# Kernel tuning notes

Hardware: AMD Instinct MI355X
Metric: run time of the kernel (lower is better)

Reference implementation:

```python
import jax, jax.numpy as jnp
import numpy as np
from math import factorial

IRREPS_IN1 = [(128, 0), (64, 1), (32, 2)]  # (mul, l): features
IRREPS_IN2 = [(1, 0), (1, 1), (1, 2)]      # spherical harmonics lmax=2
BATCH = 16384

# ---------- real Clebsch-Gordan coefficients (e3nn convention) ----------

def _su2_cg(j1, j2, j3, m1, m2, m3):
    if m3 != m1 + m2:
        return 0.0
    f = factorial
    pref = ((2 * j3 + 1) * f(j1 + j2 - j3) * f(j1 - j2 + j3) * f(-j1 + j2 + j3) / f(j1 + j2 + j3 + 1)) ** 0.5
    pref *= (f(j3 + m3) * f(j3 - m3) * f(j1 - m1) * f(j1 + m1) * f(j2 - m2) * f(j2 + m2)) ** 0.5
    s = 0.0
    for v in range(0, j1 + j2 - j3 + 1):
        a = j1 + j2 - j3 - v; b = j1 - m1 - v; c = j2 + m2 - v
        d = j3 - j2 + m1 + v; e = j3 - j1 - m2 + v
        if min(a, b, c, d, e) < 0:
            continue
        s += (-1) ** v / (f(v) * f(a) * f(b) * f(c) * f(d) * f(e))
    return pref * s


def _su2_cg_tensor(l1, l2, l3):
    C = np.zeros((2 * l1 + 1, 2 * l2 + 1, 2 * l3 + 1))
    for m1 in range(-l1, l1 + 1):
        for m2 in range(-l2, l2 + 1):
            for m3 in range(-l3, l3 + 1):
                C[l1 + m1, l2 + m2, l3 + m3] = _su2_cg(l1, l2, l3, m1, m2, m3)
    return C


def _q(l):
    # change of basis real -> complex spherical harmonics
    q = np.zeros((2 * l + 1, 2 * l + 1), dtype=np.complex128)
    for m in range(-l, 0):
        q[l + m, l + abs(m)] = 1.0 / np.sqrt(2.0)
        q[l + m, l - abs(m)] = -1j / np.sqrt(2.0)
    q[l, l] = 1.0
    for m in range(1, l + 1):
        q[l + m, l + abs(m)] = (-1) ** m / np.sqrt(2.0)
        q[l + m, l - abs(m)] = 1j * (-1) ** m / np.sqrt(2.0)
    return (-1j) ** l * q


def _real_cg(l1, l2, l3):
    C = _su2_cg_tensor(l1, l2, l3).astype(np.complex128)
    Q1, Q2, Q3 = _q(l1), _q(l2), _q(l3)
    C = np.einsum('ij,kl,mn,ikn->jlm', Q1, Q2, np.conj(Q3.T), C)
    assert np.abs(C.imag).max() < 1e-8
    return np.ascontiguousarray(C.real.astype(np.float32))

# precompute all CG tensors needed by the full tensor product
CG = {}
for _m1, _l1 in IRREPS_IN1:
    for _m2, _l2 in IRREPS_IN2:
        for _l3 in range(abs(_l1 - _l2), _l1 + _l2 + 1):
            if (_l1, _l2, _l3) not in CG:
                CG[(_l1, _l2, _l3)] = _real_cg(_l1, _l2, _l3)


def _tensor_product(x, y):
    """Full CG tensor product. x:[B,480] y:[B,9] -> dict l3 -> list of [B,mul,2l3+1]."""
    B = x.shape[0]
    outs = {}
    off1 = 0
    for mul1, l1 in IRREPS_IN1:
        d1 = 2 * l1 + 1
        x_blk = x[:, off1:off1 + mul1 * d1].reshape(B, mul1, d1)
        off1 += mul1 * d1
        off2 = 0
        for mul2, l2 in IRREPS_IN2:
            d2 = 2 * l2 + 1
            y_blk = y[:, off2:off2 + mul2 * d2].reshape(B, mul2, d2)
            off2 += mul2 * d2
            for l3 in range(abs(l1 - l2), l1 + l2 + 1):
                cg = jnp.asarray(CG[(l1, l2, l3)])  # [d1,d2,d3]
                z = jnp.einsum('ijk,bui,bvj->buvk', cg, x_blk, y_blk)
                outs.setdefault(l3, []).append(z.reshape(B, mul1 * mul2, 2 * l3 + 1))
    return outs


def setup_inputs() -> dict:
    key = jax.random.key(0)
    k = jax.random.split(key, 5)
    dim1 = sum(m * (2 * l + 1) for m, l in IRREPS_IN1)  # 480
    dim2 = sum(m * (2 * l + 1) for m, l in IRREPS_IN2)  # 9
    x = jax.random.normal(k[0], (BATCH, dim1), dtype=jnp.float32)
    y = jax.random.normal(k[1], (BATCH, dim2), dtype=jnp.float32)
    # fan-in per output l of the equivariant Linear (tp outputs with matching l)
    W0 = jax.random.normal(k[2], (224, 128), dtype=jnp.float32)
    W1 = jax.random.normal(k[3], (384, 64), dtype=jnp.float32)
    W2 = jax.random.normal(k[4], (352, 32), dtype=jnp.float32)
    return {"x": x, "y": y, "W0": W0, "W1": W1, "W2": W2}


def reference(x, y, W0, W1, W2):
    B = x.shape[0]
    outs = _tensor_product(x, y)
    Ws = {0: W0, 1: W1, 2: W2}
    res = []
    for mul_out, l in IRREPS_IN1:
        blk = jnp.concatenate(outs[l], axis=1)  # [B, tot_mul, 2l+1]
        tot_mul = blk.shape[1]
        o = jnp.einsum('bui,uv->bvi', blk, Ws[l]) / np.sqrt(tot_mul).astype(np.float32)
        res.append(o.reshape(B, mul_out * (2 * l + 1)))
    return jnp.concatenate(res, axis=1)  # [B, 480]
```

## Files before the change

kernel.cpp:

```cpp
#include <hip/hip_runtime.h>
#include <math.h>
#include <stdint.h>

#define NBATCH 16384
#define MB 16
#define NT 256
#define NBLOCKS (NBATCH/MB)
#define WT_BYTE_OFF 2560
#define XPITCH 488

typedef float  f32x4 __attribute__((ext_vector_type(4)));
typedef short  s16x8 __attribute__((ext_vector_type(8)));

__device__ const int P_CGOFF[15] = {0,1,10,35,44,53,80,125,170,245,270,315,390,415,490};
__device__ const int P_D2[15]    = {1,3,5,3,1,3,5,3,5,5,3,5,1,3,5};
__device__ const int P_D3[15]    = {1,1,1,3,3,3,3,3,3,5,5,5,5,5,5};
__device__ const int P_TSTART[15]= {0,1,4,9,12,21,30,39,54,69,74,89,104,129,154};
__device__ const int P_YOFF[15]  = {0,1,4,1,0,1,4,1,4,4,1,4,0,1,4};
__device__ const int CG_L1[15] = {0,1,2,0,1,1,1,2,2,0,1,1,2,2,2};
__device__ const int CG_L2[15] = {0,1,2,1,0,1,2,1,2,2,1,2,0,1,2};
__device__ const int CG_L3[15] = {0,0,0,1,1,1,1,1,1,2,2,2,2,2,2};

__device__ const int   SEG_WB[15] = {0,16384,24576, 28672,36864,40960,45056,49152,51200,
                                     53248,57344,59392,61440,62464,63488};
__device__ const int   SEG_SH[15] = {7,6,5, 7,6,6,6,5,5, 7,6,6,5,5,5};
__device__ const int   SEG_U0[15] = {0,128,192, 0,128,192,256,320,352, 0,128,192,256,288,320};
__device__ const int   SEG_G[15]  = {0,0,0, 1,1,1,1,1,1, 2,2,2,2,2,2};
__device__ const float SEG_SC[3]  = {0.066815310478f, 0.051031036308f, 0.053300179089f};

__device__ const float FCT[13] = {1.f,1.f,2.f,6.f,24.f,120.f,720.f,5040.f,40320.f,
                                  362880.f,3628800.f,39916800.f,479001600.f};

__device__ float su2f(int j1,int j2,int j3,int m1,int m2,int m3){
  float pref = sqrtf((float)(2*j3+1)*FCT[j1+j2-j3]*FCT[j1-j2+j3]*FCT[-j1+j2+j3]/FCT[j1+j2+j3+1]);
  pref *= sqrtf(FCT[j3+m3]*FCT[j3-m3]*FCT[j1-m1]*FCT[j1+m1]*FCT[j2-m2]*FCT[j2+m2]);
  float s = 0.f;
  for (int v=0; v<=j1+j2-j3; ++v){
    int a=j1+j2-j3-v, b=j1-m1-v, c=j2+m2-v, d=j3-j2+m1+v, e=j3-j1-m2+v;
    if (a<0||b<0||c<0||d<0||e<0) continue;
    float term = 1.f/(FCT[v]*FCT[a]*FCT[b]*FCT[c]*FCT[d]*FCT[e]);
    s += (v&1) ? -term : term;
  }
  return pref*s;
}

__device__ void qvalf(int l,int r,int c,float* qr,float* qi){
  int m = r - l;
  const float is2 = 0.70710678118654752440f;
  float br=0.f, bi=0.f;
  if (m<0){
    if (c == l - m) br = is2;
    else if (c == l + m) bi = -is2;
  } else if (m==0){
    if (c==l) br = 1.f;
  } else {
    float sg = (m&1)? -1.f : 1.f;
    if (c == l + m) br = sg*is2;
    else if (c == l - m) bi = sg*is2;
  }
  if (l==1){ float nr = bi, ni = -br; br=nr; bi=ni; }
  else if (l==2){ br=-br; bi=-bi; }
  *qr=br; *qi=bi;
}

__device__ __forceinline__ uint32_t f2bf(float f){
  uint32_t u = __float_as_uint(f);
  return (u + 0x7fffu + ((u>>16)&1u)) >> 16;
}
__device__ __forceinline__ float bf2f(uint32_t v){ return __uint_as_float(v << 16); }

__global__ void prep(const float* __restrict__ W0, const float* __restrict__ W1,
                     const float* __restrict__ W2, float* __restrict__ ws)
{
  int t = blockIdx.x*NT + threadIdx.x;
  if (t < 64512){
    uint16_t* wt = (uint16_t*)((char*)ws + WT_BYTE_OFF);
    int j = 0;
    while (j < 14 && t >= SEG_WB[j+1]) ++j;
    int idx = t - SEG_WB[j];
    int sh = SEG_SH[j];
    int v  = idx >> sh, u1 = idx & ((1<<sh)-1);
    int g  = SEG_G[j];
    int N  = (g==0)?128:(g==1)?64:32;
    const float* Wsrc = (g==0)?W0:(g==1)?W1:W2;
    wt[t] = (uint16_t)f2bf(Wsrc[(SEG_U0[j]+u1)*N + v] * SEG_SC[g]);
  }
  int t2 = t - 64512;
  if (t2 >= 0 && t2 < 615*25){
    int e = t2/25, ik = t2 - e*25;
    int i = ik/5, k = ik - (ik/5)*5;
    int p = 0;
    while (p < 14 && e >= P_CGOFF[p+1]) ++p;
    int r = e - P_CGOFF[p];
    int d2 = P_D2[p], d3 = P_D3[p];
    int i1 = r/(d2*d3); int rem = r - i1*(d2*d3);
    int i2 = rem/d3;    int i3 = rem - i2*d3;
    int l1 = CG_L1[p], l2 = CG_L2[p], l3 = CG_L3[p];
    if (i <= 2*l1 && k <= 2*l2){
      int n = i + k - l1 - l2 + l3;
      if (n >= 0 && n <= 2*l3){
        float c = su2f(l1,l2,l3, i-l1, k-l2, n-l3);
        if (c != 0.f){
          float q1r,q1i,q2r,q2i,q3r,q3i;
          qvalf(l1,i,i1,&q1r,&q1i);
          qvalf(l2,k,i2,&q2r,&q2i);
          qvalf(l3,n,i3,&q3r,&q3i);
          q3i = -q3i;
          float ar = q1r*q2r - q1i*q2i;
          float ai = q1r*q2i + q1i*q2r;
          float contrib = (ar*q3r - ai*q3i)*c;
          if (contrib != 0.f) atomicAdd(&ws[e], contrib);
        }
      }
    }
  }
}

template<int G> struct GM;
template<> struct GM<0>{
  static constexpr int NS=3, D3=1, OB=0, NMT=2, NI3=1;
  static constexpr int MUL[3]={128,64,32};
  static constexpr int D1[3] ={1,3,5};
  static constexpr int XB[3] ={0,128,320};
  static constexpr int TS[3] ={0,1,4};
  static constexpr int WB[3] ={0,16384,24576};
};
template<> struct GM<1>{
  static constexpr int NS=6, D3=3, OB=128, NMT=1, NI3=3;
  static constexpr int MUL[6]={128,64,64,64,32,32};
  static constexpr int D1[6] ={1,3,3,3,5,5};
  static constexpr int XB[6] ={0,128,128,128,320,320};
  static constexpr int TS[6] ={9,12,21,30,39,54};
  static constexpr int WB[6] ={28672,36864,40960,45056,49152,51200};
};
template<> struct GM<2>{
  static constexpr int NS=6, D3=5, OB=320, NMT=1, NI3=3;
  static constexpr int MUL[6]={128,64,64,32,32,32};
  static constexpr int D1[6] ={1,3,3,5,5,5};
  static constexpr int XB[6] ={0,128,128,320,320,320};
  static constexpr int TS[6] ={69,74,89,104,129,154};
  static constexpr int WB[6] ={53248,57344,59392,61440,62464,63488};
};

template<int G, int S, int NMT, int NI3>
__device__ __forceinline__ void do_seg(const short* __restrict__ wt,
                                       const uint16_t* __restrict__ xp,
                                       const uint16_t* __restrict__ Tsh,
                                       f32x4 (&acc)[NMT][NI3],
                                       int ln, int koct, int mt0, int i3base, int ni3)
{
  using M = GM<G>;
  constexpr int MUL = M::MUL[S];
  constexpr int KS  = MUL >> 5;
  constexpr int D1  = M::D1[S];

  s16x8 Af[NMT][KS];
  #pragma unroll
  for (int mt = 0; mt < NMT; ++mt)
    #pragma unroll
    for (int kk = 0; kk < KS; ++kk)
      Af[mt][kk] = *(const s16x8*)(wt + M::WB[S] + ((mt0+mt)*16 + ln)*MUL + kk*32 + koct);

  #pragma unroll
  for (int i1 = 0; i1 < D1; ++i1){
    s16x8 Bf[KS];
    #pragma unroll
    for (int kk = 0; kk < KS; ++kk)
      Bf[kk] = *(const s16x8*)((const short*)xp + ln*XPITCH + M::XB[S] + i1*MUL + kk*32 + koct);
    #pragma unroll
    for (int mt = 0; mt < NMT; ++mt){
      f32x4 D = {0.f,0.f,0.f,0.f};
      #pragma unroll
      for (int kk = 0; kk < KS; ++kk)
        D = __builtin_amdgcn_mfma_f32_16x16x32_bf16(Af[mt][kk], Bf[kk], D, 0, 0, 0);
      #pragma unroll
      for (int j = 0; j < NI3; ++j){
        if (j < ni3){
          const int e = M::TS[S] + i1*M::D3 + i3base + j;
          const float tv = bf2f(Tsh[e*16 + ln]);
          acc[mt][j][0] += tv*D[0];
          acc[mt][j][1] += tv*D[1];
          acc[mt][j][2] += tv*D[2];
          acc[mt][j][3] += tv*D[3];
        }
      }
    }
  }
}

template<int G>
__device__ __forceinline__ void run_group(const short* __restrict__ wt,
                                          float* __restrict__ out, int b0, int tid,
                                          const uint16_t* __restrict__ Tsh,
                                          const uint16_t* __restrict__ xp)
{
  using M = GM<G>;
  const int lane = tid & 63, w = tid >> 6;
  const int ln   = lane & 15;
  const int koct = (lane >> 4) * 8;
  constexpr int NMT = M::NMT, NI3 = M::NI3;

  int mt0, i3base, ni3;
  if constexpr (G == 0){ mt0 = 2*w; i3base = 0; ni3 = 1; }
  else if constexpr (G == 1){ mt0 = w; i3base = 0; ni3 = 3; }
  else { mt0 = w >> 1; i3base = (w & 1)*3; ni3 = (w & 1) ? 2 : 3; }

  f32x4 acc[NMT][NI3];
  #pragma unroll
  for (int a = 0; a < NMT; ++a)
    #pragma unroll
    for (int b = 0; b < NI3; ++b) acc[a][b] = (f32x4){0.f,0.f,0.f,0.f};

  do_seg<G,0,NMT,NI3>(wt, xp, Tsh, acc, ln, koct, mt0, i3base, ni3);
  do_seg<G,1,NMT,NI3>(wt, xp, Tsh, acc, ln, koct, mt0, i3base, ni3);
  do_seg<G,2,NMT,NI3>(wt, xp, Tsh, acc, ln, koct, mt0, i3base, ni3);
  if constexpr (M::NS > 3){
    do_seg<G,(M::NS>3)?3:0,NMT,NI3>(wt, xp, Tsh, acc, ln, koct, mt0, i3base, ni3);
    do_seg<G,(M::NS>4)?4:0,NMT,NI3>(wt, xp, Tsh, acc, ln, koct, mt0, i3base, ni3);
    do_seg<G,(M::NS>5)?5:0,NMT,NI3>(wt, xp, Tsh, acc, ln, koct, mt0, i3base, ni3);
  }

  const int rq = (lane >> 4) * 4;
  float* orow = out + (size_t)(b0 + ln)*480;
  if constexpr (G == 0){
    #pragma unroll
    for (int mt = 0; mt < NMT; ++mt){
      const int vb = (mt0+mt)*16 + rq;
      float4 st = make_float4(acc[mt][0][0], acc[mt][0][1], acc[mt][0][2], acc[mt][0][3]);
      *(float4*)(orow + vb) = st;
    }
  } else if constexpr (G == 1){
    const int vb = mt0*16 + rq;
    float buf[12];
    #pragma unroll
    for (int r = 0; r < 4; ++r)
      #pragma unroll
      for (int j = 0; j < 3; ++j) buf[r*3+j] = acc[0][j][r];
    float* p = orow + 128 + vb*3;
    *(float4*)(p)   = make_float4(buf[0],buf[1],buf[2],buf[3]);
    *(float4*)(p+4) = make_float4(buf[4],buf[5],buf[6],buf[7]);
    *(float4*)(p+8) = make_float4(buf[8],buf[9],buf[10],buf[11]);
  } else {
    const int vb = mt0*16 + rq;
    #pragma unroll
    for (int r = 0; r < 4; ++r)
      #pragma unroll
      for (int j = 0; j < 3; ++j)
        if (j < ni3)
          orow[320 + (vb+r)*5 + i3base + j] = acc[0][j][r];
  }
}

__device__ __forceinline__ int xmap(int c){
  if (c < 128) return c;
  if (c < 320){ int t = c - 128; int u = t/3; int i1 = t - u*3; return 128 + i1*64 + u; }
  int t = c - 320; int u = t/5; int i1 = t - u*5; return 320 + i1*32 + u;
}

__global__ __launch_bounds__(NT) void tp_linear(
    const float* __restrict__ x, const float* __restrict__ y,
    const float* __restrict__ ws, float* __restrict__ out)
{
  __shared__ __align__(16) uint16_t xp[MB*XPITCH];
  __shared__ __align__(16) uint16_t Tsh[179*16];
  __shared__ __align__(16) float    cgs[616];
  __shared__ __align__(16) float    ysm[MB*12];

  const int tid = threadIdx.x;
  const int b0 = blockIdx.x * MB;
  const short* wt = (const short*)((const char*)ws + WT_BYTE_OFF);

  for (int i = tid; i < 615; i += NT) cgs[i] = ws[i];
  for (int i = tid; i < MB*9; i += NT){
    int b = i/9, c = i - b*9;
    ysm[b*12 + c] = y[(size_t)b0*9 + i];
  }
  for (int i = tid; i < MB*120; i += NT){
    int b = i/120, q = i - b*120;
    float4 v = ((const float4*)(x + (size_t)(b0+b)*480))[q];
    int c = q*4;
    xp[b*XPITCH + xmap(c)]   = (uint16_t)f2bf(v.x);
    xp[b*XPITCH + xmap(c+1)] = (uint16_t)f2bf(v.y);
    xp[b*XPITCH + xmap(c+2)] = (uint16_t)f2bf(v.z);
    xp[b*XPITCH + xmap(c+3)] = (uint16_t)f2bf(v.w);
  }
  __syncthreads();

  for (int i = tid; i < 179*16; i += NT){
    const int e = i >> 4, b = i & 15;
    int p = 0;
    while (p < 14 && e >= P_TSTART[p+1]) ++p;
    const int r = e - P_TSTART[p];
    const int d3 = P_D3[p], d2 = P_D2[p];
    const int i1 = r / d3, j3 = r - (r/d3)*d3;
    const float* cgp = cgs + P_CGOFF[p] + (i1*d2)*d3 + j3;
    const float* yp  = ysm + b*12 + P_YOFF[p];
    float t = 0.f;
    for (int i2 = 0; i2 < d2; ++i2) t += cgp[i2*d3]*yp[i2];
    Tsh[e*16 + b] = (uint16_t)f2bf(t);
  }
  __syncthreads();

  run_group<0>(wt, out, b0, tid, Tsh, xp);
  run_group<1>(wt, out, b0, tid, Tsh, xp);
  run_group<2>(wt, out, b0, tid, Tsh, xp);
}

extern "C" void kernel_launch(void* const* d_in, const int* in_sizes, int n_in,
                              void* d_out, int out_size, void* d_ws, size_t ws_size,
                              hipStream_t stream)
{
  const float* x  = (const float*)d_in[0];
  const float* y  = (const float*)d_in[1];
  const float* W0 = (const float*)d_in[2];
  const float* W1 = (const float*)d_in[3];
  const float* W2 = (const float*)d_in[4];
  float* out = (float*)d_out;
  float* ws  = (float*)d_ws;

  hipMemsetAsync(d_ws, 0, 2464, stream);
  hipLaunchKernelGGL(prep, dim3(313), dim3(NT), 0, stream, W0, W1, W2, ws);
  hipLaunchKernelGGL(tp_linear, dim3(NBLOCKS), dim3(NT), 0, stream, x, y, ws, out);
}
```

Baseline: 135.7 us.

## Precompute CG at compile time and stage bf16 operands through output buffer

The CG coefficient tables are now built at compile time as constant memory, which removes the memset and the runtime atomic CG construction. The prep kernel also converts x to bf16 in the permuted, XOR-swizzled layout and precomputes the CG·y T values. It writes both into each block's slice of the output buffer as scratch. tp_linear then only does contiguous 16-byte loads into LDS before the MFMA work, and the MFMA loop is reordered so T scaling happens after all M-tiles. This moves per-block gather, convert and T work into a highly parallel pre-pass, at the cost of an extra round trip of about 31 MB through global memory.

```diff
diff --git a/kernel.cpp b/kernel.cpp
--- a/kernel.cpp
+++ b/kernel.cpp
@@ -7,19 +7,113 @@
 #define NT 256
 #define NBLOCKS (NBATCH/MB)
 #define WT_BYTE_OFF 2560
-#define XPITCH 488
 
 typedef float  f32x4 __attribute__((ext_vector_type(4)));
 typedef short  s16x8 __attribute__((ext_vector_type(8)));
 
-__device__ const int P_CGOFF[15] = {0,1,10,35,44,53,80,125,170,245,270,315,390,415,490};
-__device__ const int P_D2[15]    = {1,3,5,3,1,3,5,3,5,5,3,5,1,3,5};
-__device__ const int P_D3[15]    = {1,1,1,3,3,3,3,3,3,5,5,5,5,5,5};
-__device__ const int P_TSTART[15]= {0,1,4,9,12,21,30,39,54,69,74,89,104,129,154};
-__device__ const int P_YOFF[15]  = {0,1,4,1,0,1,4,1,4,4,1,4,0,1,4};
-__device__ const int CG_L1[15] = {0,1,2,0,1,1,1,2,2,0,1,1,2,2,2};
-__device__ const int CG_L2[15] = {0,1,2,1,0,1,2,1,2,2,1,2,0,1,2};
-__device__ const int CG_L3[15] = {0,0,0,1,1,1,1,1,1,2,2,2,2,2,2};
+constexpr double cfact(int n){ double r=1.0; for(int i=2;i<=n;++i) r*=(double)i; return r; }
+constexpr double csqrt_(double x){
+  if (x<=0.0) return 0.0;
+  double m=x, k=1.0;
+  while (m>1.0) { m*=0.25; k*=2.0; }
+  while (m<0.25){ m*=4.0;  k*=0.5; }
+  double g=0.7;
+  for(int i=0;i<14;++i) g = 0.5*(g + m/g);
+  return g*k;
+}
+constexpr double su2d(int j1,int j2,int j3,int m1,int m2,int m3){
+  if (m1+m2 != m3) return 0.0;
+  double pref = csqrt_((double)(2*j3+1)*cfact(j1+j2-j3)*cfact(j1-j2+j3)*cfact(-j1+j2+j3)/cfact(j1+j2+j3+1));
+  pref *= csqrt_(cfact(j3+m3)*cfact(j3-m3)*cfact(j1-m1)*cfact(j1+m1)*cfact(j2-m2)*cfact(j2+m2));
+  double s=0.0;
+  for (int v=0; v<=j1+j2-j3; ++v){
+    int a=j1+j2-j3-v, b=j1-m1-v, c=j2+m2-v, d=j3-j2+m1+v, e=j3-j1-m2+v;
+    if (a<0||b<0||c<0||d<0||e<0) continue;
+    double t = 1.0/(cfact(v)*cfact(a)*cfact(b)*cfact(c)*cfact(d)*cfact(e));
+    s += (v&1)? -t : t;
+  }
+  return pref*s;
+}
+struct C2 { double re, im; };
+constexpr C2 qvald(int l,int r,int c){
+  int m = r - l;
+  const double is2 = 0.70710678118654752440;
+  double br=0.0, bi=0.0;
+  if (m<0){ if (c==l-m) br=is2; else if (c==l+m) bi=-is2; }
+  else if (m==0){ if (c==l) br=1.0; }
+  else { double sg=(m&1)?-1.0:1.0; if (c==l+m) br=sg*is2; else if (c==l-m) bi=sg*is2; }
+  if (l==1){ double nr=bi, ni=-br; br=nr; bi=ni; }
+  else if (l==2){ br=-br; bi=-bi; }
+  return C2{br,bi};
+}
+constexpr int HP_L1[15]={0,1,2,0,1,1,1,2,2,0,1,1,2,2,2};
+constexpr int HP_L2[15]={0,1,2,1,0,1,2,1,2,2,1,2,0,1,2};
+constexpr int HP_L3[15]={0,0,0,1,1,1,1,1,1,2,2,2,2,2,2};
+constexpr int HP_CGOFF[15]={0,1,10,35,44,53,80,125,170,245,270,315,390,415,490};
+constexpr int HP_TSTART[15]={0,1,4,9,12,21,30,39,54,69,74,89,104,129,154};
+constexpr int HP_YOFF[15]={0,1,4,1,0,1,4,1,4,4,1,4,0,1,4};
+
+struct CGT { float v[616]; };
+constexpr CGT make_cg_part(int p0, int p1){
+  CGT T{};
+  for (int z=0; z<616; ++z) T.v[z]=0.f;
+  for (int p=p0; p<p1; ++p){
+    int l1=HP_L1[p], l2=HP_L2[p], l3=HP_L3[p];
+    int d1=2*l1+1, d2=2*l2+1, d3=2*l3+1;
+    double su[5][5]={};
+    for (int i=0;i<d1;++i) for (int k=0;k<d2;++k){
+      int n = i+k-l1-l2+l3;
+      su[i][k] = (n>=0 && n<d3) ? su2d(l1,l2,l3, i-l1, k-l2, n-l3) : 0.0;
+    }
+    for (int i1=0;i1<d1;++i1) for (int i2=0;i2<d2;++i2) for (int i3=0;i3<d3;++i3){
+      double val=0.0;
+      for (int i=0;i<d1;++i) for (int k=0;k<d2;++k){
+        int n = i+k-l1-l2+l3;
+        if (n<0||n>=d3) continue;
+        double c = su[i][k];
+        if (c==0.0) continue;
+        C2 q1=qvald(l1,i,i1), q2=qvald(l2,k,i2), q3=qvald(l3,n,i3);
+        double ar = q1.re*q2.re - q1.im*q2.im;
+        double ai = q1.re*q2.im + q1.im*q2.re;
+        val += (ar*q3.re + ai*q3.im)*c;
+      }
+      T.v[HP_CGOFF[p] + (i1*d2+i2)*d3 + i3] = (float)val;
+    }
+  }
+  return T;
+}
+constexpr CGT CG_A = make_cg_part(0,8);
+constexpr CGT CG_B = make_cg_part(8,12);
+constexpr CGT CG_D = make_cg_part(12,15);
+constexpr CGT cg_merge(){
+  CGT T{};
+  for (int i=0;i<616;++i) T.v[i] = CG_A.v[i] + CG_B.v[i] + CG_D.v[i];
+  return T;
+}
+__device__ __constant__ const CGT CGC = cg_merge();
+
+constexpr uint32_t make_td(int e){
+  if (e>=179) return 0u;
+  int p=0; while (p<14 && e>=HP_TSTART[p+1]) ++p;
+  int r = e - HP_TSTART[p];
+  int d2 = 2*HP_L2[p]+1, d3 = 2*HP_L3[p]+1;
+  int i1 = r/d3, j3 = r - (r/d3)*d3;
+  int base = HP_CGOFF[p] + i1*d2*d3 + j3;
+  return (uint32_t)base | ((uint32_t)d2<<10) | ((uint32_t)d3<<13) | ((uint32_t)HP_YOFF[p]<<16);
+}
+struct TDT { uint32_t v[192]; };
+constexpr TDT make_tdt(){ TDT t{}; for(int e=0;e<192;++e) t.v[e]=make_td(e); return t; }
+__device__ __constant__ const TDT TDC = make_tdt();
+
+constexpr uint16_t cmap1(int o){
+  if (o<128) return (uint16_t)o;
+  if (o<320){ int s=o-128; int i1=s>>6; int u=s&63; return (uint16_t)(128 + u*3 + i1); }
+  if (o<480){ int s=o-320; int i1=s>>5; int u=s&31; return (uint16_t)(320 + u*5 + i1); }
+  return (uint16_t)0xFFFF;
+}
+struct CMT { uint16_t v[512]; };
+constexpr CMT make_cm(){ CMT t{}; for(int o=0;o<512;++o) t.v[o]=cmap1(o); return t; }
+__device__ __constant__ const CMT CMC = make_cm();
 
 __device__ const int   SEG_WB[15] = {0,16384,24576, 28672,36864,40960,45056,49152,51200,
                                      53248,57344,59392,61440,62464,63488};
@@ -28,52 +122,19 @@
 __device__ const int   SEG_G[15]  = {0,0,0, 1,1,1,1,1,1, 2,2,2,2,2,2};
 __device__ const float SEG_SC[3]  = {0.066815310478f, 0.051031036308f, 0.053300179089f};
 
-__device__ const float FCT[13] = {1.f,1.f,2.f,6.f,24.f,120.f,720.f,5040.f,40320.f,
-                                  362880.f,3628800.f,39916800.f,479001600.f};
-
-__device__ float su2f(int j1,int j2,int j3,int m1,int m2,int m3){
-  float pref = sqrtf((float)(2*j3+1)*FCT[j1+j2-j3]*FCT[j1-j2+j3]*FCT[-j1+j2+j3]/FCT[j1+j2+j3+1]);
-  pref *= sqrtf(FCT[j3+m3]*FCT[j3-m3]*FCT[j1-m1]*FCT[j1+m1]*FCT[j2-m2]*FCT[j2+m2]);
-  float s = 0.f;
-  for (int v=0; v<=j1+j2-j3; ++v){
-    int a=j1+j2-j3-v, b=j1-m1-v, c=j2+m2-v, d=j3-j2+m1+v, e=j3-j1-m2+v;
-    if (a<0||b<0||c<0||d<0||e<0) continue;
-    float term = 1.f/(FCT[v]*FCT[a]*FCT[b]*FCT[c]*FCT[d]*FCT[e]);
-    s += (v&1) ? -term : term;
-  }
-  return pref*s;
-}
-
-__device__ void qvalf(int l,int r,int c,float* qr,float* qi){
-  int m = r - l;
-  const float is2 = 0.70710678118654752440f;
-  float br=0.f, bi=0.f;
-  if (m<0){
-    if (c == l - m) br = is2;
-    else if (c == l + m) bi = -is2;
-  } else if (m==0){
-    if (c==l) br = 1.f;
-  } else {
-    float sg = (m&1)? -1.f : 1.f;
-    if (c == l + m) br = sg*is2;
-    else if (c == l - m) bi = sg*is2;
-  }
-  if (l==1){ float nr = bi, ni = -br; br=nr; bi=ni; }
-  else if (l==2){ br=-br; bi=-bi; }
-  *qr=br; *qi=bi;
-}
-
 __device__ __forceinline__ uint32_t f2bf(float f){
   uint32_t u = __float_as_uint(f);
   return (u + 0x7fffu + ((u>>16)&1u)) >> 16;
 }
 __device__ __forceinline__ float bf2f(uint32_t v){ return __uint_as_float(v << 16); }
 
-__global__ void prep(const float* __restrict__ W0, const float* __restrict__ W1,
-                     const float* __restrict__ W2, float* __restrict__ ws)
-{
-  int t = blockIdx.x*NT + threadIdx.x;
-  if (t < 64512){
+__global__ __launch_bounds__(NT) void prep(const float* __restrict__ x, const float* __restrict__ y,
+                     const float* __restrict__ W0, const float* __restrict__ W1,
+                     const float* __restrict__ W2, float* __restrict__ ws, float* __restrict__ out)
+{
+  const int blk = blockIdx.x, tid = threadIdx.x;
+  if (blk < 252){
+    int t = blk*NT + tid;
     uint16_t* wt = (uint16_t*)((char*)ws + WT_BYTE_OFF);
     int j = 0;
     while (j < 14 && t >= SEG_WB[j+1]) ++j;
@@ -84,41 +145,43 @@
     int N  = (g==0)?128:(g==1)?64:32;
     const float* Wsrc = (g==0)?W0:(g==1)?W1:W2;
     wt[t] = (uint16_t)f2bf(Wsrc[(SEG_U0[j]+u1)*N + v] * SEG_SC[g]);
-  }
-  int t2 = t - 64512;
-  if (t2 >= 0 && t2 < 615*25){
-    int e = t2/25, ik = t2 - e*25;
-    int i = ik/5, k = ik - (ik/5)*5;
-    int p = 0;
-    while (p < 14 && e >= P_CGOFF[p+1]) ++p;
-    int r = e - P_CGOFF[p];
-    int d2 = P_D2[p], d3 = P_D3[p];
-    int i1 = r/(d2*d3); int rem = r - i1*(d2*d3);
-    int i2 = rem/d3;    int i3 = rem - i2*d3;
-    int l1 = CG_L1[p], l2 = CG_L2[p], l3 = CG_L3[p];
-    if (i <= 2*l1 && k <= 2*l2){
-      int n = i + k - l1 - l2 + l3;
-      if (n >= 0 && n <= 2*l3){
-        float c = su2f(l1,l2,l3, i-l1, k-l2, n-l3);
-        if (c != 0.f){
-          float q1r,q1i,q2r,q2i,q3r,q3i;
-          qvalf(l1,i,i1,&q1r,&q1i);
-          qvalf(l2,k,i2,&q2r,&q2i);
-          qvalf(l3,n,i3,&q3r,&q3i);
-          q3i = -q3i;
-          float ar = q1r*q2r - q1i*q2i;
-          float ai = q1r*q2i + q1i*q2r;
-          float contrib = (ar*q3r - ai*q3i)*c;
-          if (contrib != 0.f) atomicAdd(&ws[e], contrib);
-        }
-      }
-    }
+  } else if (blk < 1020){
+    int idx = (blk-252)*NT + tid;
+    const int e = idx >> 10, bblk = idx & 1023;
+    const uint32_t td = TDC.v[e];
+    const int base = td & 1023, d2 = (td>>10)&7, str = (td>>13)&7, yoff = (td>>16)&7;
+    const int b0 = bblk*16;
+    uint16_t vals[16];
+    #pragma unroll
+    for (int i=0;i<16;++i){
+      float t = 0.f;
+      for (int i2=0;i2<d2;++i2) t += CGC.v[base + i2*str] * y[(size_t)(b0+i)*9 + yoff + i2];
+      vals[i] = (uint16_t)f2bf(t);
+    }
+    char* dst = (char*)out + (size_t)bblk*30720 + 16384 + e*32;
+    *(uint4*)dst      = *(const uint4*)&vals[0];
+    *(uint4*)(dst+16) = *(const uint4*)&vals[8];
+  } else {
+    int idx = (blk-1020)*NT + tid;
+    const int b = idx >> 6, c16 = idx & 63;
+    const float* xr = x + (size_t)b*480;
+    uint16_t vals[8];
+    #pragma unroll
+    for (int jj=0;jj<8;++jj){
+      int o = c16*8 + jj;
+      uint16_t c = CMC.v[o];
+      float v = (c==0xFFFFu) ? 0.f : xr[c];
+      vals[jj] = (uint16_t)f2bf(v);
+    }
+    char* dst = (char*)out + (size_t)(b>>4)*30720 + (size_t)(b&15)*1024
+              + ((c16*16) ^ ((b&7)<<4));
+    *(uint4*)dst = *(const uint4*)&vals[0];
   }
 }
 
 template<int G> struct GM;
 template<> struct GM<0>{
-  static constexpr int NS=3, D3=1, OB=0, NMT=2, NI3=1;
+  static constexpr int NS=3, D3=1, NMT=2, NI3=1;
   static constexpr int MUL[3]={128,64,32};
   static constexpr int D1[3] ={1,3,5};
   static constexpr int XB[3] ={0,128,320};
@@ -126,7 +189,7 @@
   static constexpr int WB[3] ={0,16384,24576};
 };
 template<> struct GM<1>{
-  static constexpr int NS=6, D3=3, OB=128, NMT=1, NI3=3;
+  static constexpr int NS=6, D3=3, NMT=1, NI3=3;
   static constexpr int MUL[6]={128,64,64,64,32,32};
   static constexpr int D1[6] ={1,3,3,3,5,5};
   static constexpr int XB[6] ={0,128,128,128,320,320};
@@ -134,7 +197,7 @@
   static constexpr int WB[6] ={28672,36864,40960,45056,49152,51200};
 };
 template<> struct GM<2>{
-  static constexpr int NS=6, D3=5, OB=320, NMT=1, NI3=3;
+  static constexpr int NS=6, D3=5, NMT=1, NI3=3;
   static constexpr int MUL[6]={128,64,64,32,32,32};
   static constexpr int D1[6] ={1,3,3,5,5,5};
   static constexpr int XB[6] ={0,128,128,320,320,320};
@@ -161,27 +224,37 @@
     for (int kk = 0; kk < KS; ++kk)
       Af[mt][kk] = *(const s16x8*)(wt + M::WB[S] + ((mt0+mt)*16 + ln)*MUL + kk*32 + koct);
 
+  const int swz = (ln & 7) << 4;
+  const int koct2 = koct*2;
+  const char* xrow = (const char*)xp + ln*1024;
+
   #pragma unroll
   for (int i1 = 0; i1 < D1; ++i1){
     s16x8 Bf[KS];
     #pragma unroll
-    for (int kk = 0; kk < KS; ++kk)
-      Bf[kk] = *(const s16x8*)((const short*)xp + ln*XPITCH + M::XB[S] + i1*MUL + kk*32 + koct);
+    for (int kk = 0; kk < KS; ++kk){
+      const int cb = (M::XB[S] + i1*MUL + kk*32)*2 + koct2;
+      Bf[kk] = *(const s16x8*)(xrow + (cb ^ swz));
+    }
+    f32x4 D[NMT];
     #pragma unroll
     for (int mt = 0; mt < NMT; ++mt){
-      f32x4 D = {0.f,0.f,0.f,0.f};
+      D[mt] = (f32x4){0.f,0.f,0.f,0.f};
       #pragma unroll
       for (int kk = 0; kk < KS; ++kk)
-        D = __builtin_amdgcn_mfma_f32_16x16x32_bf16(Af[mt][kk], Bf[kk], D, 0, 0, 0);
-      #pragma unroll
-      for (int j = 0; j < NI3; ++j){
-        if (j < ni3){
-          const int e = M::TS[S] + i1*M::D3 + i3base + j;
-          const float tv = bf2f(Tsh[e*16 + ln]);
-          acc[mt][j][0] += tv*D[0];
-          acc[mt][j][1] += tv*D[1];
-          acc[mt][j][2] += tv*D[2];
-          acc[mt][j][3] += tv*D[3];
+        D[mt] = __builtin_amdgcn_mfma_f32_16x16x32_bf16(Af[mt][kk], Bf[kk], D[mt], 0, 0, 0);
+    }
+    #pragma unroll
+    for (int j = 0; j < NI3; ++j){
+      if (j < ni3){
+        const int e = M::TS[S] + i1*M::D3 + i3base + j;
+        const float tv = bf2f(Tsh[e*16 + ln]);
+        #pragma unroll
+        for (int mt = 0; mt < NMT; ++mt){
+          acc[mt][j][0] += tv*D[mt][0];
+          acc[mt][j][1] += tv*D[mt][1];
+          acc[mt][j][2] += tv*D[mt][2];
+          acc[mt][j][3] += tv*D[mt][3];
         }
       }
     }
@@ -251,53 +324,29 @@
   }
 }
 
-__device__ __forceinline__ int xmap(int c){
-  if (c < 128) return c;
-  if (c < 320){ int t = c - 128; int u = t/3; int i1 = t - u*3; return 128 + i1*64 + u; }
-  int t = c - 320; int u = t/5; int i1 = t - u*5; return 320 + i1*32 + u;
-}
-
-__global__ __launch_bounds__(NT) void tp_linear(
-    const float* __restrict__ x, const float* __restrict__ y,
-    const float* __restrict__ ws, float* __restrict__ out)
-{
-  __shared__ __align__(16) uint16_t xp[MB*XPITCH];
-  __shared__ __align__(16) uint16_t Tsh[179*16];
-  __shared__ __align__(16) float    cgs[616];
-  __shared__ __align__(16) float    ysm[MB*12];
-
+__global__ __launch_bounds__(NT) void tp_linear(const float* __restrict__ ws,
+                                                float* __restrict__ out)
+{
+  __shared__ __align__(16) uint16_t xp[MB*512];
+  __shared__ __align__(16) uint16_t Tsh[192*16];
   const int tid = threadIdx.x;
   const int b0 = blockIdx.x * MB;
   const short* wt = (const short*)((const char*)ws + WT_BYTE_OFF);
-
-  for (int i = tid; i < 615; i += NT) cgs[i] = ws[i];
-  for (int i = tid; i < MB*9; i += NT){
-    int b = i/9, c = i - b*9;
-    ysm[b*12 + c] = y[(size_t)b0*9 + i];
-  }
-  for (int i = tid; i < MB*120; i += NT){
-    int b = i/120, q = i - b*120;
-    float4 v = ((const float4*)(x + (size_t)(b0+b)*480))[q];
-    int c = q*4;
-    xp[b*XPITCH + xmap(c)]   = (uint16_t)f2bf(v.x);
-    xp[b*XPITCH + xmap(c+1)] = (uint16_t)f2bf(v.y);
-    xp[b*XPITCH + xmap(c+2)] = (uint16_t)f2bf(v.z);
-    xp[b*XPITCH + xmap(c+3)] = (uint16_t)f2bf(v.w);
-  }
-  __syncthreads();
-
-  for (int i = tid; i < 179*16; i += NT){
-    const int e = i >> 4, b = i & 15;
-    int p = 0;
-    while (p < 14 && e >= P_TSTART[p+1]) ++p;
-    const int r = e - P_TSTART[p];
-    const int d3 = P_D3[p], d2 = P_D2[p];
-    const int i1 = r / d3, j3 = r - (r/d3)*d3;
-    const float* cgp = cgs + P_CGOFF[p] + (i1*d2)*d3 + j3;
-    const float* yp  = ysm + b*12 + P_YOFF[p];
-    float t = 0.f;
-    for (int i2 = 0; i2 < d2; ++i2) t += cgp[i2*d3]*yp[i2];
-    Tsh[e*16 + b] = (uint16_t)f2bf(t);
+  const char* blkbase = (const char*)out + (size_t)blockIdx.x*30720;
+  const int wv = tid >> 6, l64 = tid & 63;
+
+  #pragma unroll
+  for (int off = 0; off < 16384; off += 4096){
+    const int a = off + wv*1024 + l64*16;
+    *(uint4*)((char*)xp + a) = *(const uint4*)(blkbase + a);
+  }
+  {
+    const int a = wv*1024 + l64*16;
+    *(uint4*)((char*)Tsh + a) = *(const uint4*)(blkbase + 16384 + a);
+  }
+  if (wv < 2){
+    const int a = 4096 + wv*1024 + l64*16;
+    *(uint4*)((char*)Tsh + a) = *(const uint4*)(blkbase + 16384 + a);
   }
   __syncthreads();
 
@@ -318,7 +367,6 @@
   float* out = (float*)d_out;
   float* ws  = (float*)d_ws;
 
-  hipMemsetAsync(d_ws, 0, 2464, stream);
-  hipLaunchKernelGGL(prep, dim3(313), dim3(NT), 0, stream, W0, W1, W2, ws);
-  hipLaunchKernelGGL(tp_linear, dim3(NBLOCKS), dim3(NT), 0, stream, x, y, ws, out);
-}
+  hipLaunchKernelGGL(prep, dim3(5116), dim3(NT), 0, stream, x, y, W0, W1, W2, ws, out);
+  hipLaunchKernelGGL(tp_linear, dim3(NBLOCKS), dim3(NT), 0, stream, ws, out);
+}
```

After: 159.9 us. 1.18x slower.
